# Kernel optimization log

Hardware: AMD Instinct MI355X
Metric: run time of the kernel (lower is better)

The kernel has to match this reference:

```python
import jax, jax.numpy as jnp
import numpy as np

D = 1024
H = 16
HD = D // H
R = 16
EPS = 1e-5


def _ln(x, w, b):
    mu = jnp.mean(x, axis=-1, keepdims=True)
    var = jnp.mean((x - mu) ** 2, axis=-1, keepdims=True)
    return (x - mu) * jax.lax.rsqrt(var + EPS) * w + b


def setup_inputs() -> dict:
    key = jax.random.key(0)
    ks = jax.random.split(key, 8)
    B, N = 32, 257
    s = 0.02
    return {
        "q_x": jax.random.normal(ks[0], (B, N, D), jnp.float32),
        "ln1_w": jnp.ones((D,), jnp.float32),
        "ln1_b": jnp.zeros((D,), jnp.float32),
        "in_proj_w": jax.random.normal(ks[1], (3 * D, D), jnp.float32) * s,
        "in_proj_b": jnp.zeros((3 * D,), jnp.float32),
        "out_w": jax.random.normal(ks[2], (D, D), jnp.float32) * s,
        "out_b": jnp.zeros((D,), jnp.float32),
        "ln2_w": jnp.ones((D,), jnp.float32),
        "ln2_b": jnp.zeros((D,), jnp.float32),
        "fc_w": jax.random.normal(ks[3], (4 * D, D), jnp.float32) * s,
        "fc_b": jnp.zeros((4 * D,), jnp.float32),
        "proj_w": jax.random.normal(ks[4], (D, 4 * D), jnp.float32) * s,
        "proj_b": jnp.zeros((D,), jnp.float32),
    }


def reference(q_x, ln1_w, ln1_b, in_proj_w, in_proj_b, out_w, out_b,
              ln2_w, ln2_b, fc_w, fc_b, proj_w, proj_b):
    B, N, _ = q_x.shape
    # --- attention (no size bias / no padding mask on first call) ---
    h = _ln(q_x, ln1_w, ln1_b)
    qkv = h @ in_proj_w.T + in_proj_b            # [B,N,3D]
    q, k, v = jnp.split(qkv, 3, axis=-1)
    to_heads = lambda t: t.reshape(B, N, H, HD).transpose(0, 2, 1, 3)  # [B,H,N,hd]
    q, k, v = to_heads(q), to_heads(k), to_heads(v)
    metric = k.mean(axis=1)                      # [B,N,hd] ToMe metric
    attn = jax.nn.softmax(jnp.einsum('bhnd,bhmd->bhnm', q, k) / np.sqrt(HD).astype(np.float32), axis=-1)
    o = jnp.einsum('bhnm,bhmd->bhnd', attn, v).transpose(0, 2, 1, 3).reshape(B, N, D)
    x = q_x + (o @ out_w.T + out_b)
    # --- ToMe: bipartite soft matching + weighted-average merge (size=None -> ones) ---
    r = min(R, (N - 1) // 2)                     # class token protected
    m = metric / jnp.linalg.norm(metric, axis=-1, keepdims=True)
    a, bm = m[:, ::2, :], m[:, 1::2, :]          # [B,Na,hd], [B,Nb,hd]
    scores = jnp.einsum('bnd,bmd->bnm', a, bm)
    scores = scores.at[:, 0, :].set(-jnp.inf)    # never merge class token
    node_max = scores.max(axis=-1)               # [B,Na]
    node_idx = scores.argmax(axis=-1)            # [B,Na]
    edge_idx = jnp.argsort(-node_max, axis=-1)   # descending similarity
    unm_idx = jnp.sort(edge_idx[:, r:], axis=-1) # keep order; cls token first
    src_idx = edge_idx[:, :r]
    dst_idx = jnp.take_along_axis(node_idx, src_idx, axis=1)  # [B,r]
    bi = jnp.arange(B)[:, None]

    def merge_sum(t):
        s, d = t[:, ::2], t[:, 1::2]
        unm = jnp.take_along_axis(s, unm_idx[:, :, None], axis=1)
        src = jnp.take_along_axis(s, src_idx[:, :, None], axis=1)
        d = d.at[bi, dst_idx].add(src)
        return jnp.concatenate([unm, d], axis=1)  # [B, N-r, C]

    size = jnp.ones((B, N, 1), x.dtype)
    x = merge_sum(x * size)
    size = merge_sum(size)
    x = x / size
    # --- MLP ---
    h2 = _ln(x, ln2_w, ln2_b)
    h2 = jax.nn.gelu(h2 @ fc_w.T + fc_b, approximate=False)
    x = x + (h2 @ proj_w.T + proj_b)
    return x
```

## Files before the change

kernel.cpp:

```cpp
#include <hip/hip_runtime.h>
#include <math.h>

#define D_ 1024
#define H_ 16
#define HD_ 64
#define BATCH 32
#define NTOK 257
#define NROWS (BATCH*NTOK)
#define NE 129
#define NO 128
#define RR 16
#define UNM 113
#define NMERGED 241
#define MROWS (BATCH*NMERGED)
#define SELSTRIDE 288

typedef unsigned short u16;
typedef unsigned int u32;
typedef __bf16 bf16x8 __attribute__((ext_vector_type(8)));
typedef float floatx4 __attribute__((ext_vector_type(4)));

__device__ __forceinline__ u16 f2bf(float f) {
    u32 u = __float_as_uint(f);
    u += 0x7fffu + ((u >> 16) & 1u);
    return (u16)(u >> 16);
}

__global__ __launch_bounds__(256) void ln_kernel(const float* __restrict__ x,
                                                 const float* __restrict__ w,
                                                 const float* __restrict__ bia,
                                                 float* __restrict__ outf,
                                                 u16* __restrict__ outb) {
    int row = blockIdx.x;
    const float* xr = x + (size_t)row * D_;
    int t = threadIdx.x;
    float v[4];
#pragma unroll
    for (int i = 0; i < 4; i++) v[i] = xr[t + 256 * i];
    float s = v[0] + v[1] + v[2] + v[3];
#pragma unroll
    for (int o = 32; o; o >>= 1) s += __shfl_down(s, o);
    __shared__ float sm[8];
    int wv = t >> 6, ln = t & 63;
    if (ln == 0) sm[wv] = s;
    __syncthreads();
    float mu = (sm[0] + sm[1] + sm[2] + sm[3]) * (1.0f / D_);
    float d0 = v[0] - mu, d1 = v[1] - mu, d2 = v[2] - mu, d3 = v[3] - mu;
    float q = d0 * d0 + d1 * d1 + d2 * d2 + d3 * d3;
#pragma unroll
    for (int o = 32; o; o >>= 1) q += __shfl_down(q, o);
    if (ln == 0) sm[4 + wv] = q;
    __syncthreads();
    float var = (sm[4] + sm[5] + sm[6] + sm[7]) * (1.0f / D_);
    float rs = rsqrtf(var + 1e-5f);
#pragma unroll
    for (int i = 0; i < 4; i++) {
        int c = t + 256 * i;
        float o = (v[i] - mu) * rs * w[c] + bia[c];
        if (outf) outf[(size_t)row * D_ + c] = o;
        if (outb) outb[(size_t)row * D_ + c] = f2bf(o);
    }
}

__global__ __launch_bounds__(256) void wm_kernel(const float* __restrict__ W,
                                                 const float* __restrict__ bias,
                                                 float* __restrict__ WmT,
                                                 float* __restrict__ bm) {
    int e = blockIdx.x * 256 + threadIdx.x;
    if (e < 64 * 1024) {
        int d = e >> 10, c = e & 1023;
        float s = 0.f;
#pragma unroll
        for (int hh = 0; hh < 16; hh++)
            s += W[(size_t)(1024 + hh * 64 + d) * 1024 + c];
        WmT[(size_t)c * 64 + d] = s * (1.0f / 16.0f);
    }
    if (e < 64) {
        float s = 0.f;
        for (int hh = 0; hh < 16; hh++) s += bias[1024 + hh * 64 + e];
        bm[e] = s * (1.0f / 16.0f);
    }
}

__global__ __launch_bounds__(256) void castw_kernel(const float* __restrict__ s0,
                                                    const float* __restrict__ s1,
                                                    const float* __restrict__ s2,
                                                    const float* __restrict__ s3,
                                                    u16* __restrict__ d0, u16* __restrict__ d1,
                                                    u16* __restrict__ d2, u16* __restrict__ d3) {
    size_t gi = ((size_t)blockIdx.x * 256 + threadIdx.x) * 8;
    const float* s; u16* d; size_t off;
    if (gi < 3145728)        { s = s0; d = d0; off = gi; }
    else if (gi < 4194304)   { s = s1; d = d1; off = gi - 3145728; }
    else if (gi < 8388608)   { s = s2; d = d2; off = gi - 4194304; }
    else                     { s = s3; d = d3; off = gi - 8388608; }
    float4 a = *(const float4*)(s + off);
    float4 b = *(const float4*)(s + off + 4);
    uint4 o;
    o.x = (u32)f2bf(a.x) | ((u32)f2bf(a.y) << 16);
    o.y = (u32)f2bf(a.z) | ((u32)f2bf(a.w) << 16);
    o.z = (u32)f2bf(b.x) | ((u32)f2bf(b.y) << 16);
    o.w = (u32)f2bf(b.z) | ((u32)f2bf(b.w) << 16);
    *(uint4*)(d + off) = o;
}

__global__ __launch_bounds__(256) void metric_kernel(const float* __restrict__ A,
                                                     const float* __restrict__ WmT,
                                                     const float* __restrict__ bm,
                                                     float* __restrict__ metric) {
    int wv = threadIdx.x >> 6, ln = threadIdx.x & 63;
    int row0 = blockIdx.x * 16 + wv * 4;
    const float* a0 = A + (size_t)row0 * 1024;
    float acc0 = 0.f, acc1 = 0.f, acc2 = 0.f, acc3 = 0.f;
    for (int k = 0; k < 1024; k += 8) {
#pragma unroll
        for (int kk = 0; kk < 8; kk++) {
            float w = WmT[(size_t)(k + kk) * 64 + ln];
            acc0 = fmaf(a0[k + kk], w, acc0);
            acc1 = fmaf(a0[1024 + k + kk], w, acc1);
            acc2 = fmaf(a0[2048 + k + kk], w, acc2);
            acc3 = fmaf(a0[3072 + k + kk], w, acc3);
        }
    }
    float b = bm[ln];
    metric[(size_t)row0 * 64 + ln] = acc0 + b;
    metric[(size_t)(row0 + 1) * 64 + ln] = acc1 + b;
    metric[(size_t)(row0 + 2) * 64 + ln] = acc2 + b;
    metric[(size_t)(row0 + 3) * 64 + ln] = acc3 + b;
}

__global__ __launch_bounds__(256) void mgemm_kernel(const u16* __restrict__ A,
                                                    const u16* __restrict__ Bw,
                                                    const float* __restrict__ bias,
                                                    const float* __restrict__ resid,
                                                    void* __restrict__ Cv,
                                                    int M, int N, int K, int mode,
                                                    int Gx) {
    __shared__ u16 As[128 * 64];
    __shared__ u16 Bs[128 * 64];
    int tid = threadIdx.x;
    int wv = tid >> 6, ln = tid & 63;
    int Gy = gridDim.x / Gx;
    int lin = blockIdx.x;
    int panelH = 8 * Gy;
    int p = lin / panelH;
    int r = lin - p * panelH;
    int xt = p * 8 + (r & 7);
    int yt = r >> 3;
    int m0 = yt * 128, n0 = xt * 128;
    int sr = wv * 8 + (ln >> 3);
    int sc = ((ln & 7) ^ (ln >> 3)) * 8;
    const u16* Ag[4]; const u16* Bg[4];
#pragma unroll
    for (int i = 0; i < 4; i++) {
        Ag[i] = A + (size_t)(m0 + i * 32 + sr) * K + sc;
        Bg[i] = Bw + (size_t)(n0 + i * 32 + sr) * K + sc;
    }
    floatx4 acc[4][4];
#pragma unroll
    for (int i = 0; i < 4; i++)
#pragma unroll
        for (int j = 0; j < 4; j++) acc[i][j] = (floatx4){0.f, 0.f, 0.f, 0.f};
    int wm = (wv & 1) * 64, wn = (wv >> 1) * 64;
    int lane16 = ln & 15, lq = ln >> 4;
    int sw = lane16 & 7;

    for (int k0 = 0; k0 < K; k0 += 64) {
        __syncthreads();
#pragma unroll
        for (int i = 0; i < 4; i++) {
            __builtin_amdgcn_global_load_lds(
                (const __attribute__((address_space(1))) void*)(Ag[i] + k0),
                (__attribute__((address_space(3))) void*)&As[i * 2048 + wv * 512], 16, 0, 0);
            __builtin_amdgcn_global_load_lds(
                (const __attribute__((address_space(1))) void*)(Bg[i] + k0),
                (__attribute__((address_space(3))) void*)&Bs[i * 2048 + wv * 512], 16, 0, 0);
        }
        __syncthreads();
#pragma unroll
        for (int ks = 0; ks < 2; ks++) {
            bf16x8 af[4], bf[4];
#pragma unroll
            for (int t = 0; t < 4; t++) {
                int slot = ((ks * 4 + lq) ^ sw) * 8;
                af[t] = *(const bf16x8*)&As[(wm + t * 16 + lane16) * 64 + slot];
                bf[t] = *(const bf16x8*)&Bs[(wn + t * 16 + lane16) * 64 + slot];
            }
#pragma unroll
            for (int mt = 0; mt < 4; mt++)
#pragma unroll
                for (int nt = 0; nt < 4; nt++)
                    acc[mt][nt] = __builtin_amdgcn_mfma_f32_16x16x32_bf16(
                        af[mt], bf[nt], acc[mt][nt], 0, 0, 0);
        }
    }
#pragma unroll
    for (int mt = 0; mt < 4; mt++) {
#pragma unroll
        for (int nt = 0; nt < 4; nt++) {
            int col = n0 + wn + nt * 16 + lane16;
            float bv = bias[col];
#pragma unroll
            for (int r2 = 0; r2 < 4; r2++) {
                int row = m0 + wm + mt * 16 + lq * 4 + r2;
                if (row < M) {
                    float v = acc[mt][nt][r2] + bv;
                    if (mode == 1) {
                        ((float*)Cv)[(size_t)row * N + col] = v + resid[(size_t)row * N + col];
                    } else {
                        if (mode == 2) v = 0.5f * v * (1.0f + erff(v * 0.70710678118654752f));
                        ((u16*)Cv)[(size_t)row * N + col] = f2bf(v);
                    }
                }
            }
        }
    }
}

#define VST 296
#define PST 40
__global__ __launch_bounds__(256, 3) void fattn_kernel(const u16* __restrict__ qkv,
                                                       u16* __restrict__ o) {
    __shared__ __align__(16) u16 Vts[64 * VST];
    __shared__ __align__(16) u16 Pb[4][16 * PST];
    int b = blockIdx.x / H_, h = blockIdx.x % H_;
    int tid = threadIdx.x;
    int wv = tid >> 6, ln = tid & 63;
    int lane16 = ln & 15, lq = ln >> 4;
    const u16* base = qkv + (size_t)b * NTOK * 3072 + h * HD_;

    for (int idx = tid; idx < NTOK * 8; idx += 256) {
        int key = idx >> 3, d0 = (idx & 7) * 8;
        uint4 u = *(const uint4*)(base + (size_t)key * 3072 + 2048 + d0);
        u16 e[8] = {(u16)u.x, (u16)(u.x >> 16), (u16)u.y, (u16)(u.y >> 16),
                    (u16)u.z, (u16)(u.z >> 16), (u16)u.w, (u16)(u.w >> 16)};
#pragma unroll
        for (int i = 0; i < 8; i++) Vts[(d0 + i) * VST + key] = e[i];
    }
    for (int idx = tid; idx < 64 * 32; idx += 256) {
        int d = idx >> 5, c = idx & 31;
        if (c) Vts[d * VST + 256 + c] = 0;
    }
    __syncthreads();

    u16* Pw = &Pb[wv][0];
    for (int qt = wv; qt < 17; qt += 4) {
        int q0 = qt * 16;
        const u16* qp = base + (size_t)(q0 + lane16) * 3072 + lq * 8;
        bf16x8 af0 = *(const bf16x8*)(qp);
        bf16x8 af1 = *(const bf16x8*)(qp + 32);
        floatx4 accs[17];
#pragma unroll
        for (int nt = 0; nt < 17; nt++) {
            const u16* kp = base + (size_t)(nt * 16 + lane16) * 3072 + 1024 + lq * 8;
            bf16x8 kb0 = *(const bf16x8*)(kp);
            bf16x8 kb1 = *(const bf16x8*)(kp + 32);
            floatx4 z = (floatx4){0.f, 0.f, 0.f, 0.f};
            z = __builtin_amdgcn_mfma_f32_16x16x32_bf16(af0, kb0, z, 0, 0, 0);
            accs[nt] = __builtin_amdgcn_mfma_f32_16x16x32_bf16(af1, kb1, z, 0, 0, 0);
        }
        if (lane16 != 0) {
#pragma unroll
            for (int r = 0; r < 4; r++) accs[16][r] = -3.0e38f;
        }
        float mrow[4], lsum[4], inv[4];
#pragma unroll
        for (int r = 0; r < 4; r++) {
            float m = -3.0e38f;
#pragma unroll
            for (int nt = 0; nt < 17; nt++) m = fmaxf(m, accs[nt][r]);
#pragma unroll
            for (int off = 1; off < 16; off <<= 1) m = fmaxf(m, __shfl_xor(m, off));
            mrow[r] = m;
            lsum[r] = 0.f;
        }
#pragma unroll
        for (int nt = 0; nt < 17; nt++) {
#pragma unroll
            for (int r = 0; r < 4; r++) {
                float p = __expf((accs[nt][r] - mrow[r]) * 0.125f);
                accs[nt][r] = p;
                lsum[r] += p;
            }
        }
#pragma unroll
        for (int r = 0; r < 4; r++) {
#pragma unroll
            for (int off = 1; off < 16; off <<= 1) lsum[r] += __shfl_xor(lsum[r], off);
            inv[r] = 1.0f / lsum[r];
        }
        floatx4 acco[4];
#pragma unroll
        for (int dt = 0; dt < 4; dt++) acco[dt] = (floatx4){0.f, 0.f, 0.f, 0.f};
#pragma unroll
        for (int ks = 0; ks < 9; ks++) {
            int nt0 = 2 * ks, nt1 = 2 * ks + 1;
#pragma unroll
            for (int r = 0; r < 4; r++) {
                float p0 = accs[nt0][r];
                float p1 = (nt1 <= 16) ? accs[nt1][r] : 0.f;
                Pw[(lq * 4 + r) * PST + lane16] = f2bf(p0);
                Pw[(lq * 4 + r) * PST + 16 + lane16] = f2bf(p1);
            }
            bf16x8 pa = *(const bf16x8*)&Pw[lane16 * PST + lq * 8];
#pragma unroll
            for (int dt = 0; dt < 4; dt++) {
                bf16x8 vb = *(const bf16x8*)&Vts[(dt * 16 + lane16) * VST + ks * 32 + lq * 8];
                acco[dt] = __builtin_amdgcn_mfma_f32_16x16x32_bf16(pa, vb, acco[dt], 0, 0, 0);
            }
        }
#pragma unroll
        for (int dt = 0; dt < 4; dt++) {
#pragma unroll
            for (int r = 0; r < 4; r++) {
                int row = q0 + lq * 4 + r;
                if (row < NTOK)
                    o[((size_t)(b * NTOK + row)) * D_ + h * HD_ + dt * 16 + lane16] =
                        f2bf(acco[dt][r] * inv[r]);
            }
        }
    }
}

__global__ __launch_bounds__(256) void mnorm_kernel(const float* __restrict__ metric,
                                                    float* __restrict__ aN,
                                                    float* __restrict__ bT) {
    int r = blockIdx.x * 4 + (threadIdx.x >> 6);
    int l = threadIdx.x & 63;
    int b = r / NTOK, t = r % NTOK;
    float v = metric[(size_t)r * 64 + l];
    float ss = v * v;
#pragma unroll
    for (int off = 1; off < 64; off <<= 1) ss += __shfl_xor(ss, off);
    float nv = v * rsqrtf(ss);
    if (!(t & 1)) aN[((size_t)b * NE + (t >> 1)) * 64 + l] = nv;
    else          bT[(size_t)b * 8192 + l * 128 + (t >> 1)] = nv;
}

__global__ __launch_bounds__(256) void score_kernel(const float* __restrict__ aN,
                                                    const float* __restrict__ bT,
                                                    float* __restrict__ nodeMax,
                                                    int* __restrict__ nodeIdx) {
    __shared__ float aL[4][64];
    int b = blockIdx.x / 33, eb = blockIdx.x % 33;
    int wv = threadIdx.x >> 6, l = threadIdx.x & 63;
    int e = eb * 4 + wv;
    if (e >= NE) return;
    aL[wv][l] = aN[((size_t)b * NE + e) * 64 + l];
    const float* bp = bT + (size_t)b * 8192;
    float s0 = 0.f, s1 = 0.f;
#pragma unroll 8
    for (int c = 0; c < 64; c++) {
        float w = aL[wv][c];
        s0 = fmaf(w, bp[c * 128 + l], s0);
        s1 = fmaf(w, bp[c * 128 + 64 + l], s1);
    }
    float bv; int bj;
    if (s1 > s0) { bv = s1; bj = l + 64; } else { bv = s0; bj = l; }
    if (e == 0) { bv = -3.0e38f; bj = 0; }
#pragma unroll
    for (int off = 1; off < 64; off <<= 1) {
        float ov = __shfl_xor(bv, off);
        int oj = __shfl_xor(bj, off);
        if (ov > bv || (ov == bv && oj < bj)) { bv = ov; bj = oj; }
    }
    if (l == 0) { nodeMax[b * NE + e] = bv; nodeIdx[b * NE + e] = bj; }
}

__global__ __launch_bounds__(64) void pick_kernel(const float* __restrict__ nodeMax,
                                                  const int* __restrict__ nodeIdx,
                                                  int* __restrict__ sel) {
    __shared__ unsigned char usedL[NE];
    __shared__ int cntL[NO];
    int b = blockIdx.x, l = threadIdx.x;
    int* sb = sel + b * SELSTRIDE;
    float v0 = nodeMax[b * NE + l];
    float v1 = nodeMax[b * NE + 64 + l];
    float v2 = (l == 0) ? nodeMax[b * NE + 128] : -3.0e38f;
    u32 usedM = (l == 0) ? 0u : 4u;
    cntL[l] = 0; cntL[l + 64] = 0;
    for (int s = 0; s < RR; s++) {
        float bv = -3.0e38f; int be = 1 << 30;
        if (!(usedM & 1u) && v0 > bv) { bv = v0; be = l; }
        if (!(usedM & 2u) && v1 > bv) { bv = v1; be = l + 64; }
        if (!(usedM & 4u) && v2 > bv) { bv = v2; be = l + 128; }
#pragma unroll
        for (int off = 1; off < 64; off <<= 1) {
            float ov = __shfl_xor(bv, off);
            int oe = __shfl_xor(be, off);
            if (ov > bv || (ov == bv && oe < be)) { bv = ov; be = oe; }
        }
        if ((be & 63) == l) usedM |= 1u << (be >> 6);
        if (l == 0) {
            sb[s] = be;
            int d = nodeIdx[b * NE + be];
            sb[16 + s] = d;
            cntL[d]++;
        }
    }
    usedL[l] = (usedM & 1u) ? 1 : 0;
    usedL[64 + l] = (usedM & 2u) ? 1 : 0;
    if (l == 0) usedL[128] = (usedM & 4u) ? 1 : 0;
    __syncthreads();
    if (l == 0) {
        int u = 0;
        for (int e = 0; e < NE; e++) if (!usedL[e]) sb[160 + u++] = e;
    }
    sb[32 + l] = cntL[l];
    sb[32 + 64 + l] = cntL[l + 64];
}

__global__ __launch_bounds__(256) void merge_kernel(const float* __restrict__ x,
                                                    const int* __restrict__ sel,
                                                    float* __restrict__ xm) {
    int blk = blockIdx.x;
    int b = blk / NMERGED, t = blk % NMERGED;
    const int* sb = sel + b * SELSTRIDE;
    int tid = threadIdx.x;
    const float* xb = x + (size_t)b * NTOK * D_;
    float* orow = xm + ((size_t)b * NMERGED + t) * D_;
    if (t < UNM) {
        int srcRow = 2 * sb[160 + t];
        const float* r = xb + (size_t)srcRow * D_;
#pragma unroll
        for (int i = 0; i < 4; i++) orow[tid + 256 * i] = r[tid + 256 * i];
    } else {
        int j = t - UNM;
        const float* r = xb + (size_t)(2 * j + 1) * D_;
        float v[4];
#pragma unroll
        for (int i = 0; i < 4; i++) v[i] = r[tid + 256 * i];
        int c = sb[32 + j];
        if (c > 0) {
            for (int s = 0; s < RR; s++) {
                if (sb[16 + s] == j) {
                    const float* rs = xb + (size_t)(2 * sb[s]) * D_;
#pragma unroll
                    for (int i = 0; i < 4; i++) v[i] += rs[tid + 256 * i];
                }
            }
            float inv = 1.0f / (float)(1 + c);
#pragma unroll
            for (int i = 0; i < 4; i++) v[i] *= inv;
        }
#pragma unroll
        for (int i = 0; i < 4; i++) orow[tid + 256 * i] = v[i];
    }
}

extern "C" void kernel_launch(void* const* d_in, const int* in_sizes, int n_in,
                              void* d_out, int out_size, void* d_ws, size_t ws_size,
                              hipStream_t stream) {
    (void)in_sizes; (void)n_in; (void)out_size; (void)ws_size;
    const float* qx   = (const float*)d_in[0];
    const float* ln1w = (const float*)d_in[1];
    const float* ln1b = (const float*)d_in[2];
    const float* ipw  = (const float*)d_in[3];
    const float* ipb  = (const float*)d_in[4];
    const float* outw = (const float*)d_in[5];
    const float* outb = (const float*)d_in[6];
    const float* ln2w = (const float*)d_in[7];
    const float* ln2b = (const float*)d_in[8];
    const float* fcw  = (const float*)d_in[9];
    const float* fcb  = (const float*)d_in[10];
    const float* pw   = (const float*)d_in[11];
    const float* pb   = (const float*)d_in[12];
    float* out = (float*)d_out;

    char* ws = (char*)d_ws;
    u16*   qkvb  = (u16*)(ws + 0);
    u16*   h2b   = (u16*)(ws + 0);
    u16*   hb    = (u16*)(ws + 51118080);
    float* hf    = (float*)(ws + 68157440);
    float* xbuf  = hf;
    u16*   ob    = (u16*)(ws + 101842944);
    float* metric= (float*)(ws + 118882304);
    float* xm    = (float*)(ws + 120987648);
    u16*   ln2bb = (u16*)(ws + 152576000);
    u16*   wqkv  = (u16*)(ws + 168566784);
    u16*   woutb = (u16*)(ws + 174858240);
    u16*   wfc   = (u16*)(ws + 176955392);
    u16*   wproj = (u16*)(ws + 185344000);
    float* WmT   = (float*)(ws + 193732608);
    float* bm    = (float*)(ws + 193994752);
    int*   sel   = (int*)(ws + 193995008);
    float* aN    = (float*)(ws + 194031872);
    float* bT    = (float*)(ws + 195088640);
    float* nMax  = (float*)(ws + 196137216);
    int*   nIdx  = (int*)(ws + 196153856);

    ln_kernel<<<NROWS, 256, 0, stream>>>(qx, ln1w, ln1b, hf, hb);
    wm_kernel<<<256, 256, 0, stream>>>(ipw, ipb, WmT, bm);
    castw_kernel<<<6144, 256, 0, stream>>>(ipw, outw, fcw, pw, wqkv, woutb, wfc, wproj);
    metric_kernel<<<514, 256, 0, stream>>>(hf, WmT, bm, metric);
    mgemm_kernel<<<24 * 65, 256, 0, stream>>>(hb, wqkv, ipb, nullptr, qkvb,
                                              NROWS, 3072, 1024, 0, 24);
    fattn_kernel<<<BATCH * H_, 256, 0, stream>>>(qkvb, ob);
    mgemm_kernel<<<8 * 65, 256, 0, stream>>>(ob, woutb, outb, qx, xbuf,
                                             NROWS, 1024, 1024, 1, 8);
    mnorm_kernel<<<2056, 256, 0, stream>>>(metric, aN, bT);
    score_kernel<<<BATCH * 33, 256, 0, stream>>>(aN, bT, nMax, nIdx);
    pick_kernel<<<BATCH, 64, 0, stream>>>(nMax, nIdx, sel);
    merge_kernel<<<BATCH * NMERGED, 256, 0, stream>>>(xbuf, sel, xm);
    ln_kernel<<<MROWS, 256, 0, stream>>>(xm, ln2w, ln2b, nullptr, ln2bb);
    mgemm_kernel<<<32 * 61, 256, 0, stream>>>(ln2bb, wfc, fcb, nullptr, h2b,
                                              MROWS, 4096, 1024, 2, 32);
    mgemm_kernel<<<8 * 61, 256, 0, stream>>>(h2b, wproj, pb, xm, out,
                                             MROWS, 1024, 4096, 1, 8);
}
```

Before: 798.8 us.

## Fuse ToMe merge with LN2, remap GEMM tiles per XCD, use tanh GELU

Merges the merge kernel and the second LayerNorm into one kernel, which saves a full read of the merged activations and one launch. The GEMM block-to-tile mapping now assigns contiguous column panels to each of the 8 XCDs (lin&7), aiming for better L2 reuse of weight tiles. It also swaps the exact erf GELU for a tanh-form approximation via __expf, which changes numerics slightly. The ln_kernel bf16 store is now unconditional, so the kernel assumes outb is always non-null.

```diff
diff --git a/kernel.cpp b/kernel.cpp
--- a/kernel.cpp
+++ b/kernel.cpp
@@ -58,7 +58,7 @@
         int c = t + 256 * i;
         float o = (v[i] - mu) * rs * w[c] + bia[c];
         if (outf) outf[(size_t)row * D_ + c] = o;
-        if (outb) outb[(size_t)row * D_ + c] = f2bf(o);
+        outb[(size_t)row * D_ + c] = f2bf(o);
     }
 }
 
@@ -140,13 +140,12 @@
     __shared__ u16 Bs[128 * 64];
     int tid = threadIdx.x;
     int wv = tid >> 6, ln = tid & 63;
-    int Gy = gridDim.x / Gx;
     int lin = blockIdx.x;
-    int panelH = 8 * Gy;
-    int p = lin / panelH;
-    int r = lin - p * panelH;
-    int xt = p * 8 + (r & 7);
-    int yt = r >> 3;
+    int pw = Gx >> 3;
+    int xcd = lin & 7;
+    int j = lin >> 3;
+    int xt = xcd * pw + (j % pw);
+    int yt = j / pw;
     int m0 = yt * 128, n0 = xt * 128;
     int sr = wv * 8 + (ln >> 3);
     int sc = ((ln & 7) ^ (ln >> 3)) * 8;
@@ -160,7 +159,7 @@
 #pragma unroll
     for (int i = 0; i < 4; i++)
 #pragma unroll
-        for (int j = 0; j < 4; j++) acc[i][j] = (floatx4){0.f, 0.f, 0.f, 0.f};
+        for (int j2 = 0; j2 < 4; j2++) acc[i][j2] = (floatx4){0.f, 0.f, 0.f, 0.f};
     int wm = (wv & 1) * 64, wn = (wv >> 1) * 64;
     int lane16 = ln & 15, lq = ln >> 4;
     int sw = lane16 & 7;
@@ -208,7 +207,10 @@
                     if (mode == 1) {
                         ((float*)Cv)[(size_t)row * N + col] = v + resid[(size_t)row * N + col];
                     } else {
-                        if (mode == 2) v = 0.5f * v * (1.0f + erff(v * 0.70710678118654752f));
+                        if (mode == 2) {
+                            float u = v * (0.7978845608028654f + 0.0356774081f * v * v);
+                            v = v / (1.0f + __expf(-2.0f * u));
+                        }
                         ((u16*)Cv)[(size_t)row * N + col] = f2bf(v);
                     }
                 }
@@ -410,24 +412,26 @@
     sb[32 + 64 + l] = cntL[l + 64];
 }
 
-__global__ __launch_bounds__(256) void merge_kernel(const float* __restrict__ x,
-                                                    const int* __restrict__ sel,
-                                                    float* __restrict__ xm) {
+__global__ __launch_bounds__(256) void merge_ln_kernel(const float* __restrict__ x,
+                                                       const int* __restrict__ sel,
+                                                       const float* __restrict__ w,
+                                                       const float* __restrict__ bia,
+                                                       float* __restrict__ xm,
+                                                       u16* __restrict__ outb) {
     int blk = blockIdx.x;
     int b = blk / NMERGED, t = blk % NMERGED;
     const int* sb = sel + b * SELSTRIDE;
     int tid = threadIdx.x;
     const float* xb = x + (size_t)b * NTOK * D_;
-    float* orow = xm + ((size_t)b * NMERGED + t) * D_;
+    float v[4];
     if (t < UNM) {
         int srcRow = 2 * sb[160 + t];
         const float* r = xb + (size_t)srcRow * D_;
 #pragma unroll
-        for (int i = 0; i < 4; i++) orow[tid + 256 * i] = r[tid + 256 * i];
+        for (int i = 0; i < 4; i++) v[i] = r[tid + 256 * i];
     } else {
         int j = t - UNM;
         const float* r = xb + (size_t)(2 * j + 1) * D_;
-        float v[4];
 #pragma unroll
         for (int i = 0; i < 4; i++) v[i] = r[tid + 256 * i];
         int c = sb[32 + j];
@@ -443,8 +447,30 @@
 #pragma unroll
             for (int i = 0; i < 4; i++) v[i] *= inv;
         }
-#pragma unroll
-        for (int i = 0; i < 4; i++) orow[tid + 256 * i] = v[i];
+    }
+    float* orow = xm + (size_t)blk * D_;
+#pragma unroll
+    for (int i = 0; i < 4; i++) orow[tid + 256 * i] = v[i];
+    float s = v[0] + v[1] + v[2] + v[3];
+#pragma unroll
+    for (int o = 32; o; o >>= 1) s += __shfl_down(s, o);
+    __shared__ float sm[8];
+    int wv = tid >> 6, ln = tid & 63;
+    if (ln == 0) sm[wv] = s;
+    __syncthreads();
+    float mu = (sm[0] + sm[1] + sm[2] + sm[3]) * (1.0f / D_);
+    float d0 = v[0] - mu, d1 = v[1] - mu, d2 = v[2] - mu, d3 = v[3] - mu;
+    float q = d0 * d0 + d1 * d1 + d2 * d2 + d3 * d3;
+#pragma unroll
+    for (int o = 32; o; o >>= 1) q += __shfl_down(q, o);
+    if (ln == 0) sm[4 + wv] = q;
+    __syncthreads();
+    float var = (sm[4] + sm[5] + sm[6] + sm[7]) * (1.0f / D_);
+    float rs = rsqrtf(var + 1e-5f);
+#pragma unroll
+    for (int i = 0; i < 4; i++) {
+        int c = tid + 256 * i;
+        outb[(size_t)blk * D_ + c] = f2bf((v[i] - mu) * rs * w[c] + bia[c]);
     }
 }
 
@@ -501,8 +527,7 @@
     mnorm_kernel<<<2056, 256, 0, stream>>>(metric, aN, bT);
     score_kernel<<<BATCH * 33, 256, 0, stream>>>(aN, bT, nMax, nIdx);
     pick_kernel<<<BATCH, 64, 0, stream>>>(nMax, nIdx, sel);
-    merge_kernel<<<BATCH * NMERGED, 256, 0, stream>>>(xbuf, sel, xm);
-    ln_kernel<<<MROWS, 256, 0, stream>>>(xm, ln2w, ln2b, nullptr, ln2bb);
+    merge_ln_kernel<<<BATCH * NMERGED, 256, 0, stream>>>(xbuf, sel, ln2w, ln2b, xm, ln2bb);
     mgemm_kernel<<<32 * 61, 256, 0, stream>>>(ln2bb, wfc, fcb, nullptr, h2b,
                                               MROWS, 4096, 1024, 2, 32);
     mgemm_kernel<<<8 * 61, 256, 0, stream>>>(h2b, wproj, pb, xm, out,
```

Measured after the change: 774.1 us. 1.03x faster.
